# Optimization experiments

Hardware: AMD Instinct MI355X
Metric: run time of the kernel (lower is better)

## Reference

```python
import jax, jax.numpy as jnp
import numpy as np

EPS = 1e-6
CHUNK = 256
N_HEADS = 16
GATE_NORM = 16.0


def rmsnorm(x, eps=EPS):
    # RMSNorm without affine; normalizes over the last axis (matches custom
    # RMSNorm applied pre-view over full dim for q/k/v and over head_dim for subln)
    return x * jax.lax.rsqrt(jnp.mean(x * x, axis=-1, keepdims=True) + eps)


def chunk_gate_retention(q, k, v, gt, chunk_size):
    """Chunked gated linear attention (RetNet/GLA-style).
    Recurrence: S_t = exp(g_t) * S_{t-1} + k_t^T v_t;  o_t = q_t @ S_t.
    q,k,v: (b,h,t,d); gt: (b,h,t) log-decay. Returns (o, last_state)."""
    b, h, t, d = q.shape
    c = chunk_size
    n = t // c
    scale = d ** -0.5
    q = q.reshape(b, h, n, c, d) * scale
    k = k.reshape(b, h, n, c, d)
    v = v.reshape(b, h, n, c, d)
    g = gt.reshape(b, h, n, c)
    bc = jnp.cumsum(g, axis=-1)            # cumulative log-decay within chunk (incl. own gate)
    B = bc[..., -1:]                        # total chunk log-decay (b,h,n,1)
    # ---- intra-chunk (causal, decayed) ----
    decay = jnp.exp(bc[..., :, None] - bc[..., None, :])  # (b,h,n,c,c), <=1 on/below diag
    mask = jnp.tril(jnp.ones((c, c), dtype=bool))
    A = jnp.einsum('bhnid,bhnjd->bhnij', q, k) * jnp.where(mask, decay, 0.0)
    o_intra = jnp.einsum('bhnij,bhnjd->bhnid', A, v)
    # ---- per-chunk kv summaries (decay from position j to chunk end) ----
    kd = k * jnp.exp(B - bc)[..., None]
    kv = jnp.einsum('bhncd,bhnce->bhnde', kd, v)          # (b,h,n,d,d)
    qd = q * jnp.exp(bc)[..., None]                        # state decay into position i
    # ---- inter-chunk recurrence over chunk index ----
    def step(S, inp):
        qd_n, kv_n, B_n = inp
        o_cross = jnp.einsum('bhcd,bhde->bhce', qd_n, S)
        S_new = jnp.exp(B_n)[..., None] * S + kv_n
        return S_new, o_cross
    S0 = jnp.zeros((b, h, d, d), dtype=q.dtype)
    inps = (jnp.moveaxis(qd, 2, 0), jnp.moveaxis(kv, 2, 0), jnp.moveaxis(B, 2, 0))
    S_last, o_cross = jax.lax.scan(step, S0, inps)
    o_cross = jnp.moveaxis(o_cross, 0, 2)                  # (b,h,n,c,d)
    o = (o_intra + o_cross).reshape(b, h, t, d)
    return o, S_last


def setup_inputs() -> dict:
    key = jax.random.key(0)
    ks = jax.random.split(key, 7)
    dim, nh = 1024, N_HEADS
    s = 0.03  # keep activations sane
    return {
        'x':   jax.random.normal(ks[0], (2, 8192, dim), dtype=jnp.float32),
        'Wq':  jax.random.normal(ks[1], (dim, dim), dtype=jnp.float32) * s,
        'Wk':  jax.random.normal(ks[2], (dim, dim), dtype=jnp.float32) * s,
        'Wv':  jax.random.normal(ks[3], (dim, dim), dtype=jnp.float32) * s,
        'Wg':  jax.random.normal(ks[4], (dim, dim), dtype=jnp.float32) * s,
        'Wgt': jax.random.normal(ks[5], (dim, nh), dtype=jnp.float32) * s,
        'Wo':  jax.random.normal(ks[6], (dim, dim), dtype=jnp.float32) * s,
    }


def reference(x, Wq, Wk, Wv, Wg, Wgt, Wo):
    b, t, dim = x.shape
    h = N_HEADS
    d = dim // h
    q = rmsnorm(x @ Wq)
    k = rmsnorm(x @ Wk)
    v = rmsnorm(x @ Wv)
    g = x @ Wg
    gt = jax.nn.log_sigmoid(x @ Wgt) / GATE_NORM   # (b,t,h)
    qr = q.reshape(b, t, h, d).transpose(0, 2, 1, 3)
    kr = k.reshape(b, t, h, d).transpose(0, 2, 1, 3)
    vr = v.reshape(b, t, h, d).transpose(0, 2, 1, 3)
    gtr = gt.transpose(0, 2, 1)                    # (b,h,t)
    o, _ = chunk_gate_retention(qr, kr, vr, gtr, CHUNK)
    o = rmsnorm(o)                                 # subln over head_dim
    o = o.transpose(0, 2, 1, 3).reshape(b, t, dim)
    o = jax.nn.silu(g) * o                         # swiglu(g, o)
    return o @ Wo
```

## Files before the change

### kernel.cpp

```cpp
#include <hip/hip_runtime.h>

#define T_SEQ 8192
#define NH 16
#define HD 64
#define DIM 1024
#define ROWS 16384
#define CHK 256
#define NCHK 32

typedef float f32x4 __attribute__((ext_vector_type(4)));
typedef __bf16 bf16x8 __attribute__((ext_vector_type(8)));
typedef short short8 __attribute__((ext_vector_type(8)));
typedef short short4v __attribute__((ext_vector_type(4)));
typedef unsigned short ushort_t;

__device__ __forceinline__ float bf2f(ushort_t u){ return __uint_as_float(((unsigned)u)<<16); }
__device__ __forceinline__ ushort_t f2bf(float f){
  unsigned u = __float_as_uint(f);
  u += 0x7FFFu + ((u>>16)&1u);
  return (ushort_t)(u>>16);
}
#define BFLO(u) __uint_as_float((u)<<16)
#define BFHI(u) __uint_as_float((u)&0xFFFF0000u)
#define MFMA16(a,b,c) __builtin_amdgcn_mfma_f32_16x16x32_bf16((a),(b),(c),0,0,0)

__global__ __launch_bounds__(256) void transpose_all(const float* __restrict__ Wq,
    const float* __restrict__ Wk, const float* __restrict__ Wv,
    const float* __restrict__ Wg, const float* __restrict__ Wo,
    ushort_t* __restrict__ wcat, ushort_t* __restrict__ wot){
  int z = blockIdx.z;
  const float* W = (z==0)?Wq:(z==1)?Wk:(z==2)?Wv:(z==3)?Wg:Wo;
  ushort_t* D = (z<4)? (wcat + (size_t)z*DIM*DIM) : wot;
  __shared__ float tile[64][65];
  int k0 = blockIdx.x*64, n0 = blockIdx.y*64;
  int tid = threadIdx.x;
  #pragma unroll
  for (int it=0; it<16; ++it){
    int idx = tid + it*256;
    int r = idx>>6, c = idx&63;
    tile[r][c] = W[(size_t)(k0+r)*DIM + n0+c];
  }
  __syncthreads();
  #pragma unroll
  for (int it=0; it<16; ++it){
    int idx = tid + it*256;
    int r = idx>>6, c = idx&63;
    D[(size_t)(n0+r)*DIM + k0+c] = f2bf(tile[c][r]);
  }
}

template<int OUT_BF16>
__global__ __launch_bounds__(256,2) void gemm_bt(const ushort_t* __restrict__ A,
    const ushort_t* __restrict__ Bt, void* __restrict__ Cv, int M, int N, int K,
    float* __restrict__ ssqp){
  __shared__ __align__(16) ushort_t As[128*64];
  __shared__ __align__(16) ushort_t Bs[128*64];
  int tid = threadIdx.x;
  int lane = tid & 63, wid = tid >> 6;
  int wr = wid >> 1, wc = wid & 1;
  int m0 = blockIdx.x * 128, n0 = blockIdx.y * 128;
  f32x4 acc[4][4] = {};
  int srow = tid >> 3;
  int sg = tid & 7;
  const int nkt = K >> 6;
  for (int kt = 0; kt < nkt; ++kt){
    short8 ra[4], rb[4];
    #pragma unroll
    for (int s = 0; s < 4; ++s){
      int row = s*32 + srow;
      int gl = sg ^ (row & 7);
      ra[s] = *(const short8*)&A[(size_t)(m0 + row)*K + kt*64 + gl*8];
      rb[s] = *(const short8*)&Bt[(size_t)(n0 + row)*K + kt*64 + gl*8];
    }
    __syncthreads();
    #pragma unroll
    for (int s = 0; s < 4; ++s){
      int row = s*32 + srow;
      *(short8*)&As[row*64 + sg*8] = ra[s];
      *(short8*)&Bs[row*64 + sg*8] = rb[s];
    }
    __syncthreads();
    #pragma unroll
    for (int kk = 0; kk < 2; ++kk){
      bf16x8 af[4], bfv[4];
      #pragma unroll
      for (int m = 0; m < 4; ++m){
        int row = wr*64 + m*16 + (lane & 15);
        int g = kk*4 + (lane >> 4);
        af[m] = *(const bf16x8*)&As[row*64 + ((g ^ (row & 7))<<3)];
      }
      #pragma unroll
      for (int n = 0; n < 4; ++n){
        int row = wc*64 + n*16 + (lane & 15);
        int g = kk*4 + (lane >> 4);
        bfv[n] = *(const bf16x8*)&Bs[row*64 + ((g ^ (row & 7))<<3)];
      }
      #pragma unroll
      for (int m = 0; m < 4; ++m)
        #pragma unroll
        for (int n = 0; n < 4; ++n)
          acc[m][n] = MFMA16(af[m], bfv[n], acc[m][n]);
    }
  }
  #pragma unroll
  for (int m = 0; m < 4; ++m){
    int row = m0 + wr*64 + m*16 + (lane>>4)*4;
    #pragma unroll
    for (int n = 0; n < 4; ++n){
      int col = n0 + wc*64 + n*16 + (lane & 15);
      #pragma unroll
      for (int r = 0; r < 4; ++r){
        float v = acc[m][n][r];
        if (OUT_BF16) ((ushort_t*)Cv)[(size_t)(row+r)*N + col] = f2bf(v);
        else          ((float*)Cv)[(size_t)(row+r)*N + col] = v;
      }
    }
  }
  if (OUT_BF16 && blockIdx.y < 24){
    int slot = blockIdx.y*2 + wc;
    #pragma unroll
    for (int m = 0; m < 4; ++m){
      #pragma unroll
      for (int r = 0; r < 4; ++r){
        float s = 0.f;
        #pragma unroll
        for (int n = 0; n < 4; ++n){ float xx = acc[m][n][r]; s += xx*xx; }
        s += __shfl_xor(s,1); s += __shfl_xor(s,2);
        s += __shfl_xor(s,4); s += __shfl_xor(s,8);
        if ((lane & 15) == 0){
          int row = m0 + wr*64 + m*16 + (lane>>4)*4 + r;
          ssqp[(size_t)slot*ROWS + row] = s;
        }
      }
    }
  }
}

__global__ __launch_bounds__(256) void rms_combine(const float* __restrict__ ssqp,
                                                   float* __restrict__ rmsb){
  int idx = blockIdx.x*256 + threadIdx.x;
  int mat = idx >> 14, row = idx & (ROWS-1);
  float s = 0.f;
  #pragma unroll
  for (int k=0;k<16;++k) s += ssqp[(size_t)(mat*16+k)*ROWS + row];
  rmsb[idx] = rsqrtf(s*(1.f/1024.f)+1e-6f);
}

__global__ __launch_bounds__(256) void gt_ker(const float* __restrict__ x,
    const float* __restrict__ Wgt, float* __restrict__ gtb, ushort_t* __restrict__ xbf){
  int row = blockIdx.x; int b = row>>13; int t = row & (T_SEQ-1);
  int tid = threadIdx.x; int lane = tid&63; int w = tid>>6;
  __shared__ float xs[1024];
  #pragma unroll
  for (int i=0;i<4;++i) xs[tid+256*i] = x[(size_t)row*DIM + tid+256*i];
  __syncthreads();
  short4v xb4;
  #pragma unroll
  for (int k2=0;k2<4;++k2) xb4[k2] = (short)f2bf(xs[tid*4+k2]);
  *(short4v*)&xbf[(size_t)row*DIM + tid*4] = xb4;
  float a0=0,a1=0,a2=0,a3=0;
  #pragma unroll
  for (int jj=0;jj<16;++jj){
    int j = lane + 64*jj;
    float xv = xs[j];
    const float* wp = &Wgt[(size_t)j*NH + w*4];
    a0 += xv*wp[0]; a1 += xv*wp[1]; a2 += xv*wp[2]; a3 += xv*wp[3];
  }
  #pragma unroll
  for (int off=32; off>=1; off>>=1){
    a0 += __shfl_xor(a0, off); a1 += __shfl_xor(a1, off);
    a2 += __shfl_xor(a2, off); a3 += __shfl_xor(a3, off);
  }
  if (lane==0){
    float za[4] = {a0,a1,a2,a3};
    #pragma unroll
    for (int i=0;i<4;++i){
      float z = za[i];
      float ls = fminf(z,0.f) - log1pf(__expf(-fabsf(z)));
      gtb[((size_t)(b*NH + w*4 + i))*T_SEQ + t] = ls * (1.f/16.f);
    }
  }
}

__global__ __launch_bounds__(512,2) void attn_p1(const ushort_t* __restrict__ qkvg,
    const float* __restrict__ gtb, const float* __restrict__ rmsb,
    float* __restrict__ Bb, ushort_t* __restrict__ kvb){
  __shared__ __align__(16) ushort_t sh2[32768];
  __shared__ float bcf[256];
  __shared__ float tmp4[4];
  ushort_t* kdt = sh2;
  ushort_t* vt  = sh2 + 16384;
  int bid = blockIdx.x; int n = bid&31; int bh = bid>>5; int b = bh>>4; int h = bh&15;
  int t0 = n*CHK; int tid = threadIdx.x; int lane = tid&63; int w = tid>>6;
  float vscan = 0.f;
  if (tid < 256){
    vscan = gtb[(size_t)bh*T_SEQ + t0 + tid];
    #pragma unroll
    for (int off=1; off<64; off<<=1){ float u = __shfl_up(vscan, off); if (lane>=off) vscan += u; }
    if (lane==63) tmp4[w] = vscan;
  }
  __syncthreads();
  float Bn = tmp4[0]+tmp4[1]+tmp4[2]+tmp4[3];
  if (tid < 256){
    float pre=0;
    #pragma unroll
    for (int i=0;i<4;++i) if (i<w) pre += tmp4[i];
    bcf[tid] = vscan + pre;
  }
  if (tid==0) Bb[bid] = Bn;
  __syncthreads();
  {
    int j = tid>>1, dh = tid&1;
    int grow = b*T_SEQ + t0 + j;
    size_t rowb = (size_t)grow*4096;
    float fk = rmsb[ROWS + grow] * __expf(Bn - bcf[j]);
    float fv = rmsb[2*ROWS + grow];
    #pragma unroll
    for (int q8=0; q8<4; ++q8){
      short8 k8 = *(const short8*)&qkvg[rowb + 1024 + h*HD + dh*32 + q8*8];
      short8 v8 = *(const short8*)&qkvg[rowb + 2048 + h*HD + dh*32 + q8*8];
      #pragma unroll
      for (int kk=0; kk<8; ++kk){
        int d = dh*32 + q8*8 + kk;
        kdt[(d<<8) + (((j>>3)^(d&7))<<3) + (j&7)] = f2bf(bf2f((ushort_t)k8[kk])*fk);
        vt [(d<<8) + (((j>>3)^(d&7))<<3) + (j&7)] = f2bf(bf2f((ushort_t)v8[kk])*fv);
      }
    }
  }
  __syncthreads();
  if (w < 4){
    f32x4 acc[4] = {};
    #pragma unroll
    for (int s=0; s<8; ++s){
      int d = w*16 + (lane&15);
      int jj = s*32 + (lane>>4)*8;
      bf16x8 ka = *(const bf16x8*)&kdt[(d<<8) + (((jj>>3)^(d&7))<<3)];
      #pragma unroll
      for (int et=0; et<4; ++et){
        int e = et*16 + (lane&15);
        bf16x8 vf = *(const bf16x8*)&vt[(e<<8) + (((jj>>3)^(e&7))<<3)];
        acc[et] = MFMA16(ka, vf, acc[et]);
      }
    }
    ushort_t* kvp = &kvb[(size_t)bid*4096];
    #pragma unroll
    for (int et=0; et<4; ++et)
      #pragma unroll
      for (int r=0; r<4; ++r)
        kvp[(et*16 + (lane&15))*64 + w*16 + (lane>>4)*4 + r] = f2bf(acc[et][r]);
  }
}

__global__ __launch_bounds__(256) void scan_ker(const ushort_t* __restrict__ kvb,
    const float* __restrict__ Bb, ushort_t* __restrict__ Sb){
  int gidx = blockIdx.x*256 + threadIdx.x;
  int bh = gidx >> 12; int f = gidx & 4095;
  float S = 0.f;
  const ushort_t* kp = &kvb[(size_t)bh*NCHK*4096 + f];
  ushort_t* sp = &Sb[(size_t)bh*NCHK*4096 + f];
  for (int n=0;n<NCHK;++n){
    sp[(size_t)n*4096] = f2bf(S);
    S = __expf(Bb[bh*NCHK+n])*S + bf2f(kp[(size_t)n*4096]);
  }
}

__global__ __launch_bounds__(512,2) void attn_p3(const ushort_t* __restrict__ qkvg,
    const float* __restrict__ gtb, const float* __restrict__ rmsb,
    const ushort_t* __restrict__ Sb, ushort_t* __restrict__ oact){
  __shared__ __align__(16) ushort_t sh[(32768+16384+1024+32+2048)/2];
  ushort_t* vt = sh;
  ushort_t* ps = sh + 16384;
  float* bcs = (float*)(sh + 24576);
  float* tmp = (float*)(sh + 25088);
  float* rqs = (float*)(sh + 25104);
  float* rks = (float*)(sh + 25616);
  int bid = blockIdx.x; int n = bid&31; int bh = bid>>5; int b = bh>>4; int h = bh&15;
  int t0 = n*CHK; int tid = threadIdx.x; int lane = tid&63; int w = tid>>6;
  int wrow = w*32;
  size_t chunkbase = (size_t)b*T_SEQ + t0;
  bf16x8 qf[2][2];
  #pragma unroll
  for (int rt=0; rt<2; ++rt)
    #pragma unroll
    for (int s=0; s<2; ++s)
      qf[rt][s] = *(const bf16x8*)&qkvg[(chunkbase + wrow + rt*16 + (lane&15))*4096
                                        + h*HD + s*32 + (lane>>4)*8];
  float vscan = 0.f;
  if (tid < 256){
    vscan = gtb[(size_t)bh*T_SEQ + t0 + tid];
    #pragma unroll
    for (int off=1; off<64; off<<=1){ float u = __shfl_up(vscan, off); if (lane>=off) vscan += u; }
    if (lane==63) tmp[w] = vscan;
  }
  __syncthreads();
  if (tid < 256){
    float pre=0;
    #pragma unroll
    for (int i=0;i<4;++i) if (i<w) pre += tmp[i];
    bcs[tid] = vscan + pre;
    int grow = b*T_SEQ + t0 + tid;
    rqs[tid] = rmsb[grow];
    rks[tid] = rmsb[ROWS + grow];
  }
  {
    int j = tid>>1, ehalf = tid&1;
    int grow = b*T_SEQ + t0 + j;
    size_t rowb = (size_t)grow*4096;
    float fv = rmsb[2*ROWS + grow];
    #pragma unroll
    for (int q8=0; q8<4; ++q8){
      short8 v8 = *(const short8*)&qkvg[rowb + 2048 + h*HD + ehalf*32 + q8*8];
      #pragma unroll
      for (int kk=0; kk<8; ++kk){
        int e = ehalf*32 + q8*8 + kk;
        vt[(e<<8) + (((j>>3)^(e&7))<<3) + (j&7)] = f2bf(bf2f((ushort_t)v8[kk])*fv);
      }
    }
  }
  __syncthreads();
  f32x4 o_[2][4] = {};
  #pragma unroll
  for (int s=0; s<2; ++s)
    #pragma unroll
    for (int et=0; et<4; ++et){
      bf16x8 stf = *(const bf16x8*)&Sb[(size_t)bid*4096 + (et*16 + (lane&15))*64
                                       + s*32 + (lane>>4)*8];
      #pragma unroll
      for (int rt=0; rt<2; ++rt)
        o_[rt][et] = MFMA16(qf[rt][s], stf, o_[rt][et]);
    }
  #pragma unroll
  for (int rt=0; rt<2; ++rt)
    #pragma unroll
    for (int rr=0; rr<4; ++rr){
      int ri = wrow + rt*16 + (lane>>4)*4 + rr;
      float fs = 0.125f*__expf(bcs[ri])*rqs[ri];
      #pragma unroll
      for (int et=0; et<4; ++et) o_[rt][et][rr] *= fs;
    }
  for (int hb=0; hb<=w; ++hb){
    int jb = hb>>1, ch = hb&1;
    int jbase = jb*64 + ch*32;
    float mb = bcs[jb*64];
    float r8[2][4];
    #pragma unroll
    for (int rt=0; rt<2; ++rt)
      #pragma unroll
      for (int rr=0; rr<4; ++rr){
        int ri = wrow + rt*16 + (lane>>4)*4 + rr;
        r8[rt][rr] = 0.125f*__expf(bcs[ri] - mb)*rqs[ri];
      }
    float c2[2];
    #pragma unroll
    for (int ct=0; ct<2; ++ct){
      int jc = jbase + ct*16 + (lane&15);
      c2[ct] = __expf(mb - bcs[jc])*rks[jc];
    }
    f32x4 s2[2][2] = {};
    #pragma unroll
    for (int s=0; s<2; ++s)
      #pragma unroll
      for (int ct=0; ct<2; ++ct){
        bf16x8 kf = *(const bf16x8*)&qkvg[(chunkbase + jbase + ct*16 + (lane&15))*4096
                                          + 1024 + h*HD + s*32 + (lane>>4)*8];
        #pragma unroll
        for (int rt=0; rt<2; ++rt)
          s2[rt][ct] = MFMA16(qf[rt][s], kf, s2[rt][ct]);
      }
    bool dia = (hb == w);
    #pragma unroll
    for (int rt=0; rt<2; ++rt)
      #pragma unroll
      for (int ct=0; ct<2; ++ct)
        #pragma unroll
        for (int rr=0; rr<4; ++rr){
          int pi = rt*16 + (lane>>4)*4 + rr;
          int pj = ct*16 + (lane&15);
          float pv = s2[rt][ct][rr] * r8[rt][rr] * c2[ct];
          if (dia && (jbase + pj) > (wrow + pi)) pv = 0.f;
          ps[w*1024 + pi*32 + (((pj>>3) ^ ((pi>>2)&3))<<3) + (pj&7)] = f2bf(pv);
        }
    bf16x8 vf[4];
    #pragma unroll
    for (int et=0; et<4; ++et){
      int e = et*16 + (lane&15);
      int jj = jbase + (lane>>4)*8;
      vf[et] = *(const bf16x8*)&vt[(e<<8) + (((jj>>3) ^ (e&7))<<3)];
    }
    bf16x8 pf[2];
    #pragma unroll
    for (int rt=0; rt<2; ++rt){
      int i = rt*16 + (lane&15);
      pf[rt] = *(const bf16x8*)&ps[w*1024 + i*32 + (((lane>>4) ^ ((i>>2)&3))<<3)];
    }
    #pragma unroll
    for (int rt=0; rt<2; ++rt)
      #pragma unroll
      for (int et=0; et<4; ++et)
        o_[rt][et] = MFMA16(pf[rt], vf[et], o_[rt][et]);
  }
  float rms8[2][4];
  #pragma unroll
  for (int rt=0; rt<2; ++rt)
    #pragma unroll
    for (int rr=0; rr<4; ++rr){
      float ssq = 0.f;
      #pragma unroll
      for (int et=0; et<4; ++et){ float xx = o_[rt][et][rr]; ssq += xx*xx; }
      ssq += __shfl_xor(ssq,1); ssq += __shfl_xor(ssq,2);
      ssq += __shfl_xor(ssq,4); ssq += __shfl_xor(ssq,8);
      rms8[rt][rr] = rsqrtf(ssq*(1.f/64.f)+1e-6f);
    }
  #pragma unroll
  for (int eh=0; eh<2; ++eh){
    #pragma unroll
    for (int rt=0; rt<2; ++rt)
      #pragma unroll
      for (int e2=0; e2<2; ++e2){
        int et = eh*2 + e2;
        #pragma unroll
        for (int rr=0; rr<4; ++rr){
          int pi = rt*16 + (lane>>4)*4 + rr;
          int pj = e2*16 + (lane&15);
          ps[w*1024 + pi*32 + (((pj>>3) ^ ((pi>>2)&3))<<3) + (pj&7)] =
            f2bf(o_[rt][et][rr]*rms8[rt][rr]);
        }
      }
    int i2 = lane&31, e16 = (lane>>5)*16;
    int gr0 = e16>>3;
    int f = (i2>>2)&3;
    short8 ov0 = *(const short8*)&ps[w*1024 + i2*32 + ((gr0^f)<<3)];
    short8 ov1 = *(const short8*)&ps[w*1024 + i2*32 + (((gr0+1)^f)<<3)];
    size_t rowg = chunkbase + wrow + i2;
    short8 gv0 = *(const short8*)&qkvg[rowg*4096 + 3072 + h*HD + eh*32 + e16];
    short8 gv1 = *(const short8*)&qkvg[rowg*4096 + 3072 + h*HD + eh*32 + e16 + 8];
    ushort_t outv[16];
    #pragma unroll
    for (int k=0;k<8;++k){
      float gf = bf2f((ushort_t)gv0[k]);
      float sg = gf/(1.f+__expf(-gf));
      outv[k] = f2bf(bf2f((ushort_t)ov0[k])*sg);
    }
    #pragma unroll
    for (int k=0;k<8;++k){
      float gf = bf2f((ushort_t)gv1[k]);
      float sg = gf/(1.f+__expf(-gf));
      outv[8+k] = f2bf(bf2f((ushort_t)ov1[k])*sg);
    }
    ushort_t* op = &oact[rowg*DIM + h*HD + eh*32 + e16];
    *(short8*)&op[0] = *(short8*)&outv[0];
    *(short8*)&op[8] = *(short8*)&outv[8];
  }
}

extern "C" void kernel_launch(void* const* d_in, const int* in_sizes, int n_in,
                              void* d_out, int out_size, void* d_ws, size_t ws_size,
                              hipStream_t stream){
  const float* x  = (const float*)d_in[0];
  const float* Wq = (const float*)d_in[1];
  const float* Wk = (const float*)d_in[2];
  const float* Wv = (const float*)d_in[3];
  const float* Wg = (const float*)d_in[4];
  const float* Wgt= (const float*)d_in[5];
  const float* Wo = (const float*)d_in[6];
  float* out = (float*)d_out;

  char* p = (char*)d_ws;
  ushort_t* xbf  = (ushort_t*)p; p += (size_t)ROWS*DIM*2;
  ushort_t* wcat = (ushort_t*)p; p += (size_t)4*DIM*DIM*2;
  ushort_t* wot  = (ushort_t*)p; p += (size_t)DIM*DIM*2;
  ushort_t* qkvg = (ushort_t*)p; p += (size_t)ROWS*4096*2;
  float* gtb = (float*)p; p += (size_t)32*T_SEQ*4;
  float* Bb  = (float*)p; p += 1024*4;
  ushort_t* kvb = (ushort_t*)p; p += (size_t)1024*4096*2;
  ushort_t* Sb = (ushort_t*)p; p += (size_t)1024*4096*2;
  ushort_t* oact = (ushort_t*)p; p += (size_t)ROWS*DIM*2;
  float* ssqp = (float*)p; p += (size_t)48*ROWS*4;
  float* rmsb = (float*)p; p += (size_t)3*ROWS*4;
  if ((size_t)(p - (char*)d_ws) > ws_size) return;

  gt_ker<<<ROWS,256,0,stream>>>(x, Wgt, gtb, xbf);
  transpose_all<<<dim3(16,16,5),256,0,stream>>>(Wq, Wk, Wv, Wg, Wo, wcat, wot);
  gemm_bt<1><<<dim3(ROWS/128, 4096/128), 256, 0, stream>>>(xbf, wcat, qkvg, ROWS, 4096, DIM, ssqp);
  rms_combine<<<(3*ROWS)/256,256,0,stream>>>(ssqp, rmsb);
  attn_p1<<<1024,512,0,stream>>>(qkvg, gtb, rmsb, Bb, kvb);
  scan_ker<<<512,256,0,stream>>>(kvb, Bb, Sb);
  attn_p3<<<1024,512,0,stream>>>(qkvg, gtb, rmsb, Sb, oact);
  gemm_bt<0><<<dim3(ROWS/128, 1024/128), 256, 0, stream>>>(oact, wot, out, ROWS, 1024, DIM, nullptr);
}
```

Baseline: 377.3 us.

## Keep attention probabilities in registers via transposed MFMA and shuffles; split QKVG GEMM

```diff
diff --git a/kernel.cpp b/kernel.cpp
--- a/kernel.cpp
+++ b/kernel.cpp
@@ -52,7 +52,7 @@
 template<int OUT_BF16>
 __global__ __launch_bounds__(256,2) void gemm_bt(const ushort_t* __restrict__ A,
     const ushort_t* __restrict__ Bt, void* __restrict__ Cv, int M, int N, int K,
-    float* __restrict__ ssqp){
+    float* __restrict__ ssqp, int yoff){
   __shared__ __align__(16) ushort_t As[128*64];
   __shared__ __align__(16) ushort_t Bs[128*64];
   int tid = threadIdx.x;
@@ -116,8 +116,8 @@
       }
     }
   }
-  if (OUT_BF16 && blockIdx.y < 24){
-    int slot = blockIdx.y*2 + wc;
+  if (OUT_BF16 && (yoff + (int)blockIdx.y) < 24){
+    int slot = (yoff + blockIdx.y)*2 + wc;
     #pragma unroll
     for (int m = 0; m < 4; ++m){
       #pragma unroll
@@ -278,13 +278,14 @@
   int t0 = n*CHK; int tid = threadIdx.x; int lane = tid&63; int w = tid>>6;
   int wrow = w*32;
   size_t chunkbase = (size_t)b*T_SEQ + t0;
+  int qcol = lane & 15, hi = lane >> 4;
   bf16x8 qf[2][2];
   #pragma unroll
   for (int rt=0; rt<2; ++rt)
     #pragma unroll
     for (int s=0; s<2; ++s)
-      qf[rt][s] = *(const bf16x8*)&qkvg[(chunkbase + wrow + rt*16 + (lane&15))*4096
-                                        + h*HD + s*32 + (lane>>4)*8];
+      qf[rt][s] = *(const bf16x8*)&qkvg[(chunkbase + wrow + rt*16 + qcol)*4096
+                                        + h*HD + s*32 + hi*8];
   float vscan = 0.f;
   if (tid < 256){
     vscan = gtb[(size_t)bh*T_SEQ + t0 + tid];
@@ -323,8 +324,7 @@
   for (int s=0; s<2; ++s)
     #pragma unroll
     for (int et=0; et<4; ++et){
-      bf16x8 stf = *(const bf16x8*)&Sb[(size_t)bid*4096 + (et*16 + (lane&15))*64
-                                       + s*32 + (lane>>4)*8];
+      bf16x8 stf = *(const bf16x8*)&Sb[(size_t)bid*4096 + (et*16 + qcol)*64 + s*32 + hi*8];
       #pragma unroll
       for (int rt=0; rt<2; ++rt)
         o_[rt][et] = MFMA16(qf[rt][s], stf, o_[rt][et]);
@@ -333,71 +333,78 @@
   for (int rt=0; rt<2; ++rt)
     #pragma unroll
     for (int rr=0; rr<4; ++rr){
-      int ri = wrow + rt*16 + (lane>>4)*4 + rr;
+      int ri = wrow + rt*16 + hi*4 + rr;
       float fs = 0.125f*__expf(bcs[ri])*rqs[ri];
       #pragma unroll
       for (int et=0; et<4; ++et) o_[rt][et][rr] *= fs;
     }
+  float rqv[2], bqv[2];
+  #pragma unroll
+  for (int rt=0; rt<2; ++rt){
+    int qr = wrow + rt*16 + qcol;
+    rqv[rt] = rqs[qr]; bqv[rt] = bcs[qr];
+  }
+  int s0 = qcol + 32*(hi&1), s1 = s0 + 16;
+  bool ctp = (hi >> 1) != 0;
   for (int hb=0; hb<=w; ++hb){
-    int jb = hb>>1, ch = hb&1;
-    int jbase = jb*64 + ch*32;
-    float mb = bcs[jb*64];
-    float r8[2][4];
-    #pragma unroll
-    for (int rt=0; rt<2; ++rt)
-      #pragma unroll
-      for (int rr=0; rr<4; ++rr){
-        int ri = wrow + rt*16 + (lane>>4)*4 + rr;
-        r8[rt][rr] = 0.125f*__expf(bcs[ri] - mb)*rqs[ri];
-      }
-    float c2[2];
-    #pragma unroll
-    for (int ct=0; ct<2; ++ct){
-      int jc = jbase + ct*16 + (lane&15);
-      c2[ct] = __expf(mb - bcs[jc])*rks[jc];
-    }
+    int jbase = hb*32;
+    bool dia = (hb == w);
+    bf16x8 kf[2][2];
+    #pragma unroll
+    for (int s=0; s<2; ++s)
+      #pragma unroll
+      for (int ct=0; ct<2; ++ct)
+        kf[s][ct] = *(const bf16x8*)&qkvg[(chunkbase + jbase + ct*16 + qcol)*4096
+                                          + 1024 + h*HD + s*32 + hi*8];
     f32x4 s2[2][2] = {};
     #pragma unroll
     for (int s=0; s<2; ++s)
       #pragma unroll
-      for (int ct=0; ct<2; ++ct){
-        bf16x8 kf = *(const bf16x8*)&qkvg[(chunkbase + jbase + ct*16 + (lane&15))*4096
-                                          + 1024 + h*HD + s*32 + (lane>>4)*8];
+      for (int ct=0; ct<2; ++ct)
         #pragma unroll
         for (int rt=0; rt<2; ++rt)
-          s2[rt][ct] = MFMA16(qf[rt][s], kf, s2[rt][ct]);
-      }
-    bool dia = (hb == w);
-    #pragma unroll
-    for (int rt=0; rt<2; ++rt)
-      #pragma unroll
-      for (int ct=0; ct<2; ++ct)
+          s2[rt][ct] = MFMA16(kf[s][ct], qf[rt][s], s2[rt][ct]);
+    bf16x8 vf[4];
+    #pragma unroll
+    for (int et=0; et<4; ++et){
+      int e = et*16 + qcol;
+      int jj = jbase + hi*8;
+      vf[et] = *(const bf16x8*)&vt[(e<<8) + (((jj>>3) ^ (e&7))<<3)];
+    }
+    #pragma unroll
+    for (int rt=0; rt<2; ++rt){
+      int qr = wrow + rt*16 + qcol;
+      unsigned wd[2][2];
+      #pragma unroll
+      for (int ct=0; ct<2; ++ct){
+        float pv[4];
         #pragma unroll
         for (int rr=0; rr<4; ++rr){
-          int pi = rt*16 + (lane>>4)*4 + rr;
-          int pj = ct*16 + (lane&15);
-          float pv = s2[rt][ct][rr] * r8[rt][rr] * c2[ct];
-          if (dia && (jbase + pj) > (wrow + pi)) pv = 0.f;
-          ps[w*1024 + pi*32 + (((pj>>3) ^ ((pi>>2)&3))<<3) + (pj&7)] = f2bf(pv);
+          int kr = jbase + ct*16 + hi*4 + rr;
+          float val = s2[rt][ct][rr] * 0.125f * rqv[rt] * rks[kr] * __expf(bqv[rt] - bcs[kr]);
+          if (dia && kr > qr) val = 0.f;
+          pv[rr] = val;
         }
-    bf16x8 vf[4];
-    #pragma unroll
-    for (int et=0; et<4; ++et){
-      int e = et*16 + (lane&15);
-      int jj = jbase + (lane>>4)*8;
-      vf[et] = *(const bf16x8*)&vt[(e<<8) + (((jj>>3) ^ (e&7))<<3)];
-    }
-    bf16x8 pf[2];
-    #pragma unroll
-    for (int rt=0; rt<2; ++rt){
-      int i = rt*16 + (lane&15);
-      pf[rt] = *(const bf16x8*)&ps[w*1024 + i*32 + (((lane>>4) ^ ((i>>2)&3))<<3)];
-    }
-    #pragma unroll
-    for (int rt=0; rt<2; ++rt)
+        wd[ct][0] = ((unsigned)f2bf(pv[1])<<16) | f2bf(pv[0]);
+        wd[ct][1] = ((unsigned)f2bf(pv[3])<<16) | f2bf(pv[2]);
+      }
+      unsigned a00 = (unsigned)__shfl((int)wd[0][0], s0);
+      unsigned a10 = (unsigned)__shfl((int)wd[1][0], s0);
+      unsigned a01 = (unsigned)__shfl((int)wd[0][1], s0);
+      unsigned a11 = (unsigned)__shfl((int)wd[1][1], s0);
+      unsigned b00 = (unsigned)__shfl((int)wd[0][0], s1);
+      unsigned b10 = (unsigned)__shfl((int)wd[1][0], s1);
+      unsigned b01 = (unsigned)__shfl((int)wd[0][1], s1);
+      unsigned b11 = (unsigned)__shfl((int)wd[1][1], s1);
+      union { unsigned u[4]; bf16x8 v; } pa;
+      pa.u[0] = ctp ? a10 : a00;
+      pa.u[1] = ctp ? a11 : a01;
+      pa.u[2] = ctp ? b10 : b00;
+      pa.u[3] = ctp ? b11 : b01;
       #pragma unroll
       for (int et=0; et<4; ++et)
-        o_[rt][et] = MFMA16(pf[rt], vf[et], o_[rt][et]);
+        o_[rt][et] = MFMA16(pa.v, vf[et], o_[rt][et]);
+    }
   }
   float rms8[2][4];
   #pragma unroll
@@ -420,8 +427,8 @@
         int et = eh*2 + e2;
         #pragma unroll
         for (int rr=0; rr<4; ++rr){
-          int pi = rt*16 + (lane>>4)*4 + rr;
-          int pj = e2*16 + (lane&15);
+          int pi = rt*16 + hi*4 + rr;
+          int pj = e2*16 + qcol;
           ps[w*1024 + pi*32 + (((pj>>3) ^ ((pi>>2)&3))<<3) + (pj&7)] =
             f2bf(o_[rt][et][rr]*rms8[rt][rr]);
         }
@@ -481,10 +488,12 @@
 
   gt_ker<<<ROWS,256,0,stream>>>(x, Wgt, gtb, xbf);
   transpose_all<<<dim3(16,16,5),256,0,stream>>>(Wq, Wk, Wv, Wg, Wo, wcat, wot);
-  gemm_bt<1><<<dim3(ROWS/128, 4096/128), 256, 0, stream>>>(xbf, wcat, qkvg, ROWS, 4096, DIM, ssqp);
+  gemm_bt<1><<<dim3(ROWS/128, 16), 256, 0, stream>>>(xbf, wcat, qkvg, ROWS, 4096, DIM, ssqp, 0);
+  gemm_bt<1><<<dim3(ROWS/128, 16), 256, 0, stream>>>(xbf, wcat + (size_t)2048*DIM,
+                                                     qkvg + 2048, ROWS, 4096, DIM, ssqp, 16);
   rms_combine<<<(3*ROWS)/256,256,0,stream>>>(ssqp, rmsb);
   attn_p1<<<1024,512,0,stream>>>(qkvg, gtb, rmsb, Bb, kvb);
   scan_ker<<<512,256,0,stream>>>(kvb, Bb, Sb);
   attn_p3<<<1024,512,0,stream>>>(qkvg, gtb, rmsb, Sb, oact);
-  gemm_bt<0><<<dim3(ROWS/128, 1024/128), 256, 0, stream>>>(oact, wot, out, ROWS, 1024, DIM, nullptr);
-}
+  gemm_bt<0><<<dim3(ROWS/128, 1024/128), 256, 0, stream>>>(oact, wot, out, ROWS, 1024, DIM, nullptr, 0);
+}
```

Result: no change. 384.1 us (+1.8%).
